# Kernel optimization log

Measured on AMD Instinct MI355X. Metric: run time of the kernel, lower is better.

## Reference

```python
import jax, jax.numpy as jnp
import numpy as np

B, C_IN, H, W = 4, 256, 64, 64
LATENT = 256


def setup_inputs() -> dict:
    key = jax.random.key(0)
    ks = jax.random.split(key, 12)
    s_in = 1.0 / np.sqrt(C_IN)
    s_lat = 1.0 / np.sqrt(LATENT)
    return {
        "x": jax.random.normal(ks[0], (B, C_IN, H, W), dtype=jnp.float32),
        # 1x1 conv weights stored as [out, in]
        "wq": jax.random.normal(ks[1], (LATENT, C_IN), dtype=jnp.float32) * s_in,
        "bq": jnp.zeros((LATENT,), dtype=jnp.float32),
        "wk": jax.random.normal(ks[2], (LATENT, C_IN), dtype=jnp.float32) * s_in,
        "bk": jnp.zeros((LATENT,), dtype=jnp.float32),
        "wv": jax.random.normal(ks[3], (LATENT, C_IN), dtype=jnp.float32) * s_in,
        "bv": jnp.zeros((LATENT,), dtype=jnp.float32),
        "w_out": jax.random.normal(ks[4], (C_IN, LATENT), dtype=jnp.float32) * s_lat,
        "b_out": jnp.zeros((C_IN,), dtype=jnp.float32),
        # positional-embedding MLP (torch nn.Linear: y = x @ W.T + b)
        "mlp_w1": jax.random.normal(ks[5], (LATENT, LATENT), dtype=jnp.float32) * s_lat,
        "mlp_b1": jnp.zeros((LATENT,), dtype=jnp.float32),
        "mlp_w2": jax.random.normal(ks[6], (LATENT, LATENT), dtype=jnp.float32) * s_lat,
        "mlp_b2": jnp.zeros((LATENT,), dtype=jnp.float32),
    }


def _sinusoidal_table(timesteps, dim):
    # embed[t, d] = sin(arg) if d even else cos(arg), arg = t / 10000**(2d/dim)
    t = jnp.arange(timesteps, dtype=jnp.float32)[:, None]
    p = jnp.arange(dim, dtype=jnp.float32)[None, :]
    w = t / jnp.power(jnp.float32(10000.0), 2.0 * p / dim)
    even = (jnp.arange(dim) % 2 == 0)[None, :]
    return jnp.where(even, jnp.sin(w), jnp.cos(w))  # [T, dim]


def _conv1x1(x, w, b):
    # x: [B, Cin, H, W], w: [Cout, Cin]
    return jnp.einsum('bchw,oc->bohw', x, w) + b[None, :, None, None]


def reference(x, wq, bq, wk, bk, wv, bv, w_out, b_out, mlp_w1, mlp_b1, mlp_w2, mlp_b2):
    batch, _, h, w_ = x.shape
    L = wq.shape[0]
    hw = h * w_

    q = _conv1x1(x, wq, bq)
    k = _conv1x1(x, wk, bk)
    v = _conv1x1(x, wv, bv)

    pe = _sinusoidal_table(hw, L)                     # [HW, L]
    pe = jax.nn.silu(pe @ mlp_w1.T + mlp_b1) @ mlp_w2.T + mlp_b2
    pe = pe.reshape(1, L, h, w_)                      # faithful to torch reshape

    q = (q + pe).reshape(batch, L, hw)
    k = (k + pe).reshape(batch, L, hw)
    v = (v + pe).reshape(batch, L, hw)

    # attention[b, i, j] = sum_c q[b, c, i] * k[b, c, j] / sqrt(L)
    att = jnp.einsum('bci,bcj->bij', q, k) / jnp.sqrt(jnp.float32(L))
    att = jax.nn.softmax(att, axis=1)                 # SAGAN-style: softmax over queries
    res = jnp.einsum('bci,bij->bcj', v, att)          # bmm(v, attention)
    res = res.reshape(batch, L, h, w_)
    return _conv1x1(res, w_out, b_out)
```

## Files before the change

kernel.cpp:

```cpp
#include <hip/hip_runtime.h>
#include <cstdint>


typedef short s8v __attribute__((ext_vector_type(8)));
typedef float f32x4 __attribute__((ext_vector_type(4)));
typedef unsigned int u32x2 __attribute__((ext_vector_type(2)));
typedef unsigned int u32x4 __attribute__((ext_vector_type(4)));

#define DEVI static __device__ __forceinline__

DEVI unsigned short f2bf(float f) {
  union { float f; uint32_t u; } x; x.f = f;
  uint32_t u = x.u;
  return (unsigned short)((u + 0x7fffu + ((u >> 16) & 1u)) >> 16);
}

DEVI void pl32swap(uint32_t& a, uint32_t& b) {
#if __has_builtin(__builtin_amdgcn_permlane32_swap)
  u32x2 r = __builtin_amdgcn_permlane32_swap(a, b, false, false);
  a = r[0]; b = r[1];
#else
  asm("v_permlane32_swap_b32 %0, %1" : "+v"(a), "+v"(b));
#endif
}

DEVI void gl_lds16(const void* g, void* l) {
  __builtin_amdgcn_global_load_lds(
      (const __attribute__((address_space(1))) void*)g,
      (__attribute__((address_space(3))) void*)l,
      16, 0, 0);
}

DEVI void stage(const unsigned short* src, int ld, unsigned short* lds, int t) {
  gl_lds16(src + (long)(t >> 2) * ld + (t & 3) * 8, lds + (t >> 6) * 512);
}

template <int OBF, int BIAS, int PEM, int SILU>
__global__ __launch_bounds__(256) void gemm_nt(
    const unsigned short* __restrict__ A, const unsigned short* __restrict__ B,
    void* __restrict__ Cp, int K, int N, int ld, long sA, long sB, long sC,
    const float* __restrict__ bias, const float* __restrict__ pe, float scale) {
  const int bz = blockIdx.z;
  const unsigned short* Ab = A + (long)bz * sA;
  const unsigned short* Bb = B + (long)bz * sB;
  const int m0 = blockIdx.x * 128, n0 = blockIdx.y * 128;
  __shared__ __align__(16) unsigned short As[4096], Bs[4096];
  const int t = threadIdx.x;
  const int wave = t >> 6, lane = t & 63;
  const int wr = wave >> 1, wc = wave & 1;

  f32x4 acc[4][4];
#pragma unroll
  for (int i = 0; i < 4; i++)
#pragma unroll
    for (int j = 0; j < 4; j++) acc[i][j] = f32x4{0.f, 0.f, 0.f, 0.f};

  const int rl = lane & 15, kp = (lane >> 4) * 8;

  for (int k0 = 0; k0 < K; k0 += 32) {
    stage(Ab + (long)m0 * ld + k0, ld, As, t);
    stage(Ab + (long)(m0 + 64) * ld + k0, ld, As + 2048, t);
    stage(Bb + (long)n0 * ld + k0, ld, Bs, t);
    stage(Bb + (long)(n0 + 64) * ld + k0, ld, Bs + 2048, t);
    __syncthreads();

    s8v af[4], bfr[4];
#pragma unroll
    for (int i = 0; i < 4; i++)
      af[i] = *(const s8v*)(As + (wr * 64 + i * 16 + rl) * 32 + kp);
#pragma unroll
    for (int j = 0; j < 4; j++)
      bfr[j] = *(const s8v*)(Bs + (wc * 64 + j * 16 + rl) * 32 + kp);
#pragma unroll
    for (int i = 0; i < 4; i++)
#pragma unroll
      for (int j = 0; j < 4; j++)
        acc[i][j] = __builtin_amdgcn_mfma_f32_16x16x32_bf16(af[i], bfr[j],
                                                            acc[i][j], 0, 0, 0);
    __syncthreads();
  }

  const long cb = (long)bz * sC;
#pragma unroll
  for (int i = 0; i < 4; i++) {
    const int r0 = m0 + wr * 64 + i * 16 + (lane >> 4) * 4;
#pragma unroll
    for (int j = 0; j < 4; j++) {
      const int col = n0 + wc * 64 + j * 16 + (lane & 15);
#pragma unroll
      for (int r = 0; r < 4; r++) {
        const int row = r0 + r;
        float val = acc[i][j][r] * scale;
        if (BIAS == 1) val += bias[row];
        if (BIAS == 2) val += bias[col];
        if (PEM == 1) val += pe[(long)row * 4096 + col];
        if (PEM == 2) val += pe[(long)col * 4096 + row];
        if (SILU) val = val / (1.0f + __expf(-val));
        const long ci = cb + (long)row * N + col;
        if (OBF)
          ((unsigned short*)Cp)[ci] = f2bf(val);
        else
          ((float*)Cp)[ci] = val;
      }
    }
  }
}

__global__ __launch_bounds__(256) void gemm_qk(
    const unsigned short* __restrict__ XT, const unsigned short* __restrict__ wqb,
    const unsigned short* __restrict__ wkb, unsigned short* __restrict__ qT,
    unsigned short* __restrict__ kT, const float* __restrict__ bq,
    const float* __restrict__ bk, const float* __restrict__ pe) {
  const int bz = blockIdx.z;
  const unsigned short* Ab = XT + (long)bz * 1048576;
  const int m0 = blockIdx.x * 128, n0 = blockIdx.y * 128;
  __shared__ __align__(16) unsigned short As[4096], Bq[4096], Bk[4096];
  const int t = threadIdx.x;
  const int wave = t >> 6, lane = t & 63;
  const int wr = wave >> 1, wc = wave & 1;

  f32x4 aq[4][4], ak[4][4];
#pragma unroll
  for (int i = 0; i < 4; i++)
#pragma unroll
    for (int j = 0; j < 4; j++) {
      aq[i][j] = f32x4{0.f, 0.f, 0.f, 0.f};
      ak[i][j] = f32x4{0.f, 0.f, 0.f, 0.f};
    }

  const int rl = lane & 15, kp = (lane >> 4) * 8;

  for (int k0 = 0; k0 < 256; k0 += 32) {
    stage(Ab + (long)m0 * 256 + k0, 256, As, t);
    stage(Ab + (long)(m0 + 64) * 256 + k0, 256, As + 2048, t);
    stage(wqb + (long)n0 * 256 + k0, 256, Bq, t);
    stage(wqb + (long)(n0 + 64) * 256 + k0, 256, Bq + 2048, t);
    stage(wkb + (long)n0 * 256 + k0, 256, Bk, t);
    stage(wkb + (long)(n0 + 64) * 256 + k0, 256, Bk + 2048, t);
    __syncthreads();

    s8v af[4], bq4[4], bk4[4];
#pragma unroll
    for (int i = 0; i < 4; i++)
      af[i] = *(const s8v*)(As + (wr * 64 + i * 16 + rl) * 32 + kp);
#pragma unroll
    for (int j = 0; j < 4; j++) {
      bq4[j] = *(const s8v*)(Bq + (wc * 64 + j * 16 + rl) * 32 + kp);
      bk4[j] = *(const s8v*)(Bk + (wc * 64 + j * 16 + rl) * 32 + kp);
    }
#pragma unroll
    for (int i = 0; i < 4; i++)
#pragma unroll
      for (int j = 0; j < 4; j++) {
        aq[i][j] = __builtin_amdgcn_mfma_f32_16x16x32_bf16(af[i], bq4[j],
                                                           aq[i][j], 0, 0, 0);
        ak[i][j] = __builtin_amdgcn_mfma_f32_16x16x32_bf16(af[i], bk4[j],
                                                           ak[i][j], 0, 0, 0);
      }
    __syncthreads();
  }

  const long cb = (long)bz * 1048576;
#pragma unroll
  for (int i = 0; i < 4; i++) {
    const int r0 = m0 + wr * 64 + i * 16 + (lane >> 4) * 4;
#pragma unroll
    for (int j = 0; j < 4; j++) {
      const int col = n0 + wc * 64 + j * 16 + (lane & 15);
#pragma unroll
      for (int r = 0; r < 4; r++) {
        const int row = r0 + r;
        const float p = pe[(long)col * 4096 + row];
        qT[cb + (long)row * 256 + col] = f2bf(aq[i][j][r] + bq[col] + p);
        kT[cb + (long)row * 256 + col] = f2bf(ak[i][j][r] + bk[col] + p);
      }
    }
  }
}

__global__ __launch_bounds__(256) void gemm_out_f(
    const unsigned short* __restrict__ wob, const float* __restrict__ oPart,
    const float* __restrict__ lPart, const float* __restrict__ bo,
    float* __restrict__ out) {
  const int bz = blockIdx.z;
  const int m0 = blockIdx.x * 128, n0 = blockIdx.y * 128;
  __shared__ __align__(16) unsigned short As[4096], Bs[4096];
  const int t = threadIdx.x;
  const int wave = t >> 6, lane = t & 63;
  const int wr = wave >> 1, wc = wave & 1;

  f32x4 acc[4][4];
#pragma unroll
  for (int i = 0; i < 4; i++)
#pragma unroll
    for (int j = 0; j < 4; j++) acc[i][j] = f32x4{0.f, 0.f, 0.f, 0.f};

  const int rl = lane & 15, kp = (lane >> 4) * 8;
  const int tr = t >> 2, tc8 = (t & 3) * 8;

  const int j0_ = n0 + tr, j1_ = n0 + 64 + tr;
  const float* l0p = lPart + (long)(bz * 2) * 4096;
  const float* l1p = lPart + (long)(bz * 2 + 1) * 4096;
  const float inv0 = 1.0f / (l0p[j0_] + l1p[j0_]);
  const float inv1 = 1.0f / (l0p[j1_] + l1p[j1_]);
  const float* oP0 = oPart + (long)(bz * 2) * 1048576;
  const float* oP1 = oPart + (long)(bz * 2 + 1) * 1048576;

  for (int k0 = 0; k0 < 256; k0 += 32) {
    stage(wob + (long)m0 * 256 + k0, 256, As, t);
    stage(wob + (long)(m0 + 64) * 256 + k0, 256, As + 2048, t);
#pragma unroll
    for (int h = 0; h < 2; h++) {
      const int j = h ? j1_ : j0_;
      const float inv = h ? inv1 : inv0;
      const float4* a4 = (const float4*)(oP0 + (long)j * 256 + k0 + tc8);
      const float4* d4 = (const float4*)(oP1 + (long)j * 256 + k0 + tc8);
      const float4 a0 = a4[0], a1 = a4[1], d0 = d4[0], d1 = d4[1];
      s8v pk;
      pk[0] = (short)f2bf((a0.x + d0.x) * inv);
      pk[1] = (short)f2bf((a0.y + d0.y) * inv);
      pk[2] = (short)f2bf((a0.z + d0.z) * inv);
      pk[3] = (short)f2bf((a0.w + d0.w) * inv);
      pk[4] = (short)f2bf((a1.x + d1.x) * inv);
      pk[5] = (short)f2bf((a1.y + d1.y) * inv);
      pk[6] = (short)f2bf((a1.z + d1.z) * inv);
      pk[7] = (short)f2bf((a1.w + d1.w) * inv);
      *(s8v*)(Bs + h * 2048 + tr * 32 + tc8) = pk;
    }
    __syncthreads();

    s8v af[4], bfr[4];
#pragma unroll
    for (int i = 0; i < 4; i++)
      af[i] = *(const s8v*)(As + (wr * 64 + i * 16 + rl) * 32 + kp);
#pragma unroll
    for (int j = 0; j < 4; j++)
      bfr[j] = *(const s8v*)(Bs + (wc * 64 + j * 16 + rl) * 32 + kp);
#pragma unroll
    for (int i = 0; i < 4; i++)
#pragma unroll
      for (int j = 0; j < 4; j++)
        acc[i][j] = __builtin_amdgcn_mfma_f32_16x16x32_bf16(af[i], bfr[j],
                                                            acc[i][j], 0, 0, 0);
    __syncthreads();
  }

  const long cb = (long)bz * 1048576;
#pragma unroll
  for (int i = 0; i < 4; i++) {
    const int r0 = m0 + wr * 64 + i * 16 + (lane >> 4) * 4;
#pragma unroll
    for (int j = 0; j < 4; j++) {
      const int col = n0 + wc * 64 + j * 16 + (lane & 15);
#pragma unroll
      for (int r = 0; r < 4; r++) {
        const int row = r0 + r;
        out[cb + (long)row * 4096 + col] = acc[i][j][r] + bo[row];
      }
    }
  }
}

__global__ __launch_bounds__(512, 2) void flash_attn(
    const unsigned short* __restrict__ qTp, const unsigned short* __restrict__ kTp,
    const unsigned short* __restrict__ vBp, float* __restrict__ oPart,
    float* __restrict__ lPart) {
  const int bid = blockIdx.x;
  const int xcd = bid & 7;
  const int b = xcd >> 1, ihalf = xcd & 1;
  const int j0 = (bid >> 3) * 128;
  const long S = 1048576;
  const long ibase = (long)ihalf * 2048;
  const unsigned short* q = qTp + (long)b * S;
  const unsigned short* k = kTp + (long)b * S;
  const unsigned short* v = vBp + (long)b * S;
  const int ob = b * 2 + ihalf;

  __shared__ __align__(16) unsigned char ldsb[131584];

  const int t = threadIdx.x;
  const int wave = t >> 6, lane = t & 63;
  const int jq = wave & 3, ch = wave >> 2;
  const int rl = lane & 15, g = lane >> 4;
  const int kp = g * 8;
  const int ksw = ((g ^ ((rl >> 1) & 3)) << 3);
  const int qrow = (rl & 3) | ((rl & 4) << 1) | ((rl & 8) >> 1);
  const int kswq = ((g ^ ((qrow >> 1) & 3)) << 3);
  const int th = t >> 8, tt = t & 255;

  const unsigned short* krow = k + (long)(j0 + jq * 32 + rl) * 256 + kp;
  s8v kreg[2][8];
#pragma unroll
  for (int jf = 0; jf < 2; jf++)
#pragma unroll
    for (int s = 0; s < 8; s++)
      kreg[jf][s] = *(const s8v*)(krow + jf * 16 * 256 + s * 32);

  f32x4 oacc[16][2];
#pragma unroll
  for (int cf = 0; cf < 16; cf++)
#pragma unroll
    for (int jf = 0; jf < 2; jf++) oacc[cf][jf] = f32x4{0.f, 0.f, 0.f, 0.f};
  float plsum[2] = {0.f, 0.f};

  const int tr = tt >> 2, tc = tt & 3;
  const int sc = (tc ^ ((tr >> 1) & 3)) * 8;
  const unsigned short* qsrc[4];
  const unsigned short* vsrc[4];
  const int dsto = (tt >> 6) * 512;
#pragma unroll
  for (int ss = 0; ss < 4; ss++) {
    const int s_ = ss * 2 + th;
    qsrc[ss] = q + ibase * 256 + s_ * 32 + (long)tr * 256 + sc;
    vsrc[ss] = v + (long)((s_ >> 1) * 64) * 4096 + ibase + (s_ & 1) * 32 +
               (long)tr * 4096 + sc;
  }

#define STAGE_QV(bufsel)                                                     \
  {                                                                          \
    unsigned short* qD = (unsigned short*)(ldsb + ((bufsel) << 15));         \
    unsigned short* vD = (unsigned short*)(ldsb + 65536 + ((bufsel) << 15)); \
    _Pragma("unroll") for (int ss = 0; ss < 4; ss++) {                       \
      const int s_ = ss * 2 + th;                                            \
      gl_lds16(qsrc[ss], qD + s_ * 2048 + dsto);                             \
      gl_lds16(vsrc[ss], vD + s_ * 2048 + dsto);                             \
      qsrc[ss] += 16384;                                                     \
      vsrc[ss] += 64;                                                        \
    }                                                                        \
  }

  STAGE_QV(0)

  for (int n = 0; n < 32; ++n) {
    const int cur = n & 1;
    __syncthreads();
    STAGE_QV(cur ^ 1)

    f32x4 sa[2][2];
#pragma unroll
    for (int kk = 0; kk < 2; kk++)
#pragma unroll
      for (int jf = 0; jf < 2; jf++) sa[kk][jf] = f32x4{0.f, 0.f, 0.f, 0.f};
    const unsigned short* qbase =
        (const unsigned short*)(ldsb + (cur << 15)) +
        (ch * 32 + qrow) * 32 + kswq;
#pragma unroll
    for (int s = 0; s < 8; s++) {
      s8v qf0 = *(const s8v*)(qbase + s * 2048);
      s8v qf1 = *(const s8v*)(qbase + s * 2048 + 512);
      sa[0][0] = __builtin_amdgcn_mfma_f32_16x16x32_bf16(qf0, kreg[0][s],
                                                         sa[0][0], 0, 0, 0);
      sa[0][1] = __builtin_amdgcn_mfma_f32_16x16x32_bf16(qf0, kreg[1][s],
                                                         sa[0][1], 0, 0, 0);
      sa[1][0] = __builtin_amdgcn_mfma_f32_16x16x32_bf16(qf1, kreg[0][s],
                                                         sa[1][0], 0, 0, 0);
      sa[1][1] = __builtin_amdgcn_mfma_f32_16x16x32_bf16(qf1, kreg[1][s],
                                                         sa[1][1], 0, 0, 0);
    }

    uint32_t pd[2][2][2];
#pragma unroll
    for (int kk = 0; kk < 2; kk++)
#pragma unroll
      for (int jf = 0; jf < 2; jf++) {
        const float p0 = exp2f(sa[kk][jf][0] * 0.09016844005556021f);
        const float p1 = exp2f(sa[kk][jf][1] * 0.09016844005556021f);
        const float p2 = exp2f(sa[kk][jf][2] * 0.09016844005556021f);
        const float p3 = exp2f(sa[kk][jf][3] * 0.09016844005556021f);
        plsum[jf] += (p0 + p1) + (p2 + p3);
        pd[kk][jf][0] = (uint32_t)f2bf(p0) | ((uint32_t)f2bf(p1) << 16);
        pd[kk][jf][1] = (uint32_t)f2bf(p2) | ((uint32_t)f2bf(p3) << 16);
      }

    s8v pB[2];
#pragma unroll
    for (int jf = 0; jf < 2; jf++) {
      uint32_t a0 = pd[0][jf][0], b0 = pd[1][jf][0];
      uint32_t a1 = pd[0][jf][1], b1 = pd[1][jf][1];
      pl32swap(a0, b0);
      pl32swap(a1, b1);
      u32x4 w4 = {a0, a1, b0, b1};
      pB[jf] = __builtin_bit_cast(s8v, w4);
    }

    const unsigned short* vbase =
        (const unsigned short*)(ldsb + 65536 + (cur << 15)) + ch * 2048 +
        rl * 32 + ksw;
#pragma unroll
    for (int cf = 0; cf < 16; cf++) {
      s8v vb = *(const s8v*)(vbase + (cf >> 2) * 4096 + (cf & 3) * 512);
      oacc[cf][0] = __builtin_amdgcn_mfma_f32_16x16x32_bf16(vb, pB[0],
                                                            oacc[cf][0], 0, 0, 0);
      oacc[cf][1] = __builtin_amdgcn_mfma_f32_16x16x32_bf16(vb, pB[1],
                                                            oacc[cf][1], 0, 0, 0);
    }
  }

#pragma unroll
  for (int jf = 0; jf < 2; jf++) {
    plsum[jf] += __shfl_xor(plsum[jf], 16);
    plsum[jf] += __shfl_xor(plsum[jf], 32);
  }

  __syncthreads();
  float4* ex = (float4*)ldsb;
  float* exl = (float*)(ldsb + 131072);
  if (ch == 1) {
#pragma unroll
    for (int jf = 0; jf < 2; jf++) {
#pragma unroll
      for (int cf = 0; cf < 16; cf++)
        ex[jq * 2048 + (jf * 16 + rl) * 64 + cf * 4 + g] =
            float4{oacc[cf][jf][0], oacc[cf][jf][1], oacc[cf][jf][2],
                   oacc[cf][jf][3]};
      if (g == 0) exl[jq * 32 + jf * 16 + rl] = plsum[jf];
    }
  }
  __syncthreads();
  if (ch == 0) {
    float4* op4 = (float4*)(oPart + (long)ob * 1048576);
#pragma unroll
    for (int jf = 0; jf < 2; jf++) {
      const int jl = jq * 32 + jf * 16 + rl;
      if (g == 0)
        lPart[(long)ob * 4096 + j0 + jl] = plsum[jf] + exl[jl];
#pragma unroll
      for (int cf = 0; cf < 16; cf++) {
        const float4 o = ex[jq * 2048 + (jf * 16 + rl) * 64 + cf * 4 + g];
        op4[(long)(j0 + jl) * 64 + cf * 4 + g] =
            float4{oacc[cf][jf][0] + o.x, oacc[cf][jf][1] + o.y,
                   oacc[cf][jf][2] + o.z, oacc[cf][jf][3] + o.w};
      }
    }
  }
#undef STAGE_QV
}

__global__ __launch_bounds__(256) void convert6(
    const float* __restrict__ a0, const float* __restrict__ a1,
    const float* __restrict__ a2, const float* __restrict__ a3,
    const float* __restrict__ a4, const float* __restrict__ a5,
    unsigned short* __restrict__ dst) {
  int idx = blockIdx.x * 256 + threadIdx.x;
  int m = idx >> 16, r = idx & 65535;
  const float* s;
  switch (m) {
    case 0: s = a0; break;
    case 1: s = a1; break;
    case 2: s = a2; break;
    case 3: s = a3; break;
    case 4: s = a4; break;
    default: s = a5; break;
  }
  dst[idx] = f2bf(s[r]);
}

__global__ __launch_bounds__(256) void embed_k(unsigned short* __restrict__ e) {
  int idx = blockIdx.x * 256 + threadIdx.x;
  int t = idx >> 8, d = idx & 255;
  float freq = exp2f((float)d * -0.10381025296573598f);
  float w = (float)t * freq;
  float s, c;
  __sincosf(w, &s, &c);
  e[idx] = f2bf((d & 1) ? c : s);
}

__global__ void transpose_x(const float* __restrict__ x,
                            unsigned short* __restrict__ xt) {
  __shared__ float tile[32][33];
  const int b = blockIdx.z;
  const int s0 = blockIdx.x * 32, c0 = blockIdx.y * 32;
  const int tx = threadIdx.x, ty = threadIdx.y;
  const float* xb = x + (long)b * 256 * 4096;
#pragma unroll
  for (int r = 0; r < 32; r += 8)
    tile[ty + r][tx] = xb[(long)(c0 + ty + r) * 4096 + s0 + tx];
  __syncthreads();
  unsigned short* xtb = xt + (long)b * 4096 * 256;
#pragma unroll
  for (int r = 0; r < 32; r += 8)
    xtb[(long)(s0 + ty + r) * 256 + c0 + tx] = f2bf(tile[tx][ty + r]);
}

extern "C" void kernel_launch(void* const* d_in, const int* in_sizes, int n_in,
                              void* d_out, int out_size, void* d_ws,
                              size_t ws_size, hipStream_t stream) {
  const float* x  = (const float*)d_in[0];
  const float* wq = (const float*)d_in[1];
  const float* bq = (const float*)d_in[2];
  const float* wk = (const float*)d_in[3];
  const float* bk = (const float*)d_in[4];
  const float* wv = (const float*)d_in[5];
  const float* bv = (const float*)d_in[6];
  const float* wo = (const float*)d_in[7];
  const float* bo = (const float*)d_in[8];
  const float* w1 = (const float*)d_in[9];
  const float* b1 = (const float*)d_in[10];
  const float* w2 = (const float*)d_in[11];
  const float* b2 = (const float*)d_in[12];
  float* out = (float*)d_out;

  char* ws = (char*)d_ws;
  unsigned short* wqb = (unsigned short*)(ws + 0);
  unsigned short* wkb = (unsigned short*)(ws + 131072);
  unsigned short* wvb = (unsigned short*)(ws + 262144);
  unsigned short* wob = (unsigned short*)(ws + 393216);
  unsigned short* w1b = (unsigned short*)(ws + 524288);
  unsigned short* w2b = (unsigned short*)(ws + 655360);
  unsigned short* emb = (unsigned short*)(ws + 786432);
  unsigned short* h1b = (unsigned short*)(ws + 2883584);
  float*          peF = (float*)(ws + 4980736);
  unsigned short* XT  = (unsigned short*)(ws + 9175040);
  unsigned short* qT  = (unsigned short*)(ws + 17563648);
  unsigned short* kT  = (unsigned short*)(ws + 25952256);
  unsigned short* vB  = (unsigned short*)(ws + 34340864);
  float*          oP  = (float*)(ws + 51118080);
  float*          lP  = (float*)(ws + 84672512);
  (void)ws_size; (void)in_sizes; (void)n_in; (void)out_size;

  const dim3 B256(256);
  const long S = 1048576;

  convert6<<<1536, B256, 0, stream>>>(wq, wk, wv, wo, w1, w2, wqb);
  embed_k<<<4096, B256, 0, stream>>>(emb);
  gemm_nt<1, 2, 0, 1><<<dim3(32, 2, 1), B256, 0, stream>>>(
      emb, w1b, h1b, 256, 256, 256, 0, 0, 0, b1, nullptr, 1.0f);
  gemm_nt<0, 2, 0, 0><<<dim3(32, 2, 1), B256, 0, stream>>>(
      h1b, w2b, peF, 256, 256, 256, 0, 0, 0, b2, nullptr, 1.0f);
  transpose_x<<<dim3(128, 8, 4), dim3(32, 8), 0, stream>>>(x, XT);
  gemm_qk<<<dim3(32, 2, 4), B256, 0, stream>>>(XT, wqb, wkb, qT, kT, bq, bk,
                                               peF);
  gemm_nt<1, 1, 1, 0><<<dim3(2, 32, 4), B256, 0, stream>>>(
      wvb, XT, vB, 256, 4096, 256, 0, S, S, bv, peF, 1.0f);

  flash_attn<<<256, dim3(512), 0, stream>>>(qT, kT, vB, oP, lP);

  gemm_out_f<<<dim3(2, 32, 4), B256, 0, stream>>>(wob, oP, lP, bo, out);
}
```

Before: 162.0 us.

## Fuse V projection into QK GEMM and merge prep kernels into one launch

The V projection GEMM now shares the staged X tile with Q and K inside one 512-thread kernel. Each wave computes a 64x32 slice of all three outputs, and V is written transposed with packed ushort4 stores. The weight conversion, sinusoidal embedding and x transpose kernels are merged into one launch that picks its work by block index. This removes redundant reads of X and cuts launch overhead, in exchange for more LDS and register use per block.

```diff
diff --git a/kernel.cpp b/kernel.cpp
--- a/kernel.cpp
+++ b/kernel.cpp
@@ -106,56 +106,62 @@
   }
 }
 
-__global__ __launch_bounds__(256) void gemm_qk(
+__global__ __launch_bounds__(512) void gemm_qkv(
     const unsigned short* __restrict__ XT, const unsigned short* __restrict__ wqb,
-    const unsigned short* __restrict__ wkb, unsigned short* __restrict__ qT,
-    unsigned short* __restrict__ kT, const float* __restrict__ bq,
-    const float* __restrict__ bk, const float* __restrict__ pe) {
+    const unsigned short* __restrict__ wkb, const unsigned short* __restrict__ wvb,
+    unsigned short* __restrict__ qT, unsigned short* __restrict__ kT,
+    unsigned short* __restrict__ vB, const float* __restrict__ bq,
+    const float* __restrict__ bk, const float* __restrict__ bv,
+    const float* __restrict__ pe) {
   const int bz = blockIdx.z;
   const unsigned short* Ab = XT + (long)bz * 1048576;
   const int m0 = blockIdx.x * 128, n0 = blockIdx.y * 128;
-  __shared__ __align__(16) unsigned short As[4096], Bq[4096], Bk[4096];
+  __shared__ __align__(16) unsigned short As[4096], Bq[4096], Bk[4096],
+      Bv[4096];
   const int t = threadIdx.x;
   const int wave = t >> 6, lane = t & 63;
-  const int wr = wave >> 1, wc = wave & 1;
-
-  f32x4 aq[4][4], ak[4][4];
+  const int wm = wave >> 2, wn = wave & 3;
+  const int rl = lane & 15, kp = (lane >> 4) * 8;
+  const int th = t >> 8, tt = t & 255;
+
+  f32x4 aq[4][2], ak[4][2], av[4][2];
 #pragma unroll
   for (int i = 0; i < 4; i++)
 #pragma unroll
-    for (int j = 0; j < 4; j++) {
+    for (int j = 0; j < 2; j++) {
       aq[i][j] = f32x4{0.f, 0.f, 0.f, 0.f};
       ak[i][j] = f32x4{0.f, 0.f, 0.f, 0.f};
-    }
-
-  const int rl = lane & 15, kp = (lane >> 4) * 8;
+      av[i][j] = f32x4{0.f, 0.f, 0.f, 0.f};
+    }
 
   for (int k0 = 0; k0 < 256; k0 += 32) {
-    stage(Ab + (long)m0 * 256 + k0, 256, As, t);
-    stage(Ab + (long)(m0 + 64) * 256 + k0, 256, As + 2048, t);
-    stage(wqb + (long)n0 * 256 + k0, 256, Bq, t);
-    stage(wqb + (long)(n0 + 64) * 256 + k0, 256, Bq + 2048, t);
-    stage(wkb + (long)n0 * 256 + k0, 256, Bk, t);
-    stage(wkb + (long)(n0 + 64) * 256 + k0, 256, Bk + 2048, t);
-    __syncthreads();
-
-    s8v af[4], bq4[4], bk4[4];
+    const long ro = (long)(th * 64) * 256 + k0;
+    stage(Ab + (long)m0 * 256 + ro, 256, As + th * 2048, tt);
+    stage(wqb + (long)n0 * 256 + ro, 256, Bq + th * 2048, tt);
+    stage(wkb + (long)n0 * 256 + ro, 256, Bk + th * 2048, tt);
+    stage(wvb + (long)n0 * 256 + ro, 256, Bv + th * 2048, tt);
+    __syncthreads();
+
+    s8v af[4], b0[2], b1[2], b2[2];
 #pragma unroll
     for (int i = 0; i < 4; i++)
-      af[i] = *(const s8v*)(As + (wr * 64 + i * 16 + rl) * 32 + kp);
-#pragma unroll
-    for (int j = 0; j < 4; j++) {
-      bq4[j] = *(const s8v*)(Bq + (wc * 64 + j * 16 + rl) * 32 + kp);
-      bk4[j] = *(const s8v*)(Bk + (wc * 64 + j * 16 + rl) * 32 + kp);
+      af[i] = *(const s8v*)(As + (wm * 64 + i * 16 + rl) * 32 + kp);
+#pragma unroll
+    for (int j = 0; j < 2; j++) {
+      b0[j] = *(const s8v*)(Bq + (wn * 32 + j * 16 + rl) * 32 + kp);
+      b1[j] = *(const s8v*)(Bk + (wn * 32 + j * 16 + rl) * 32 + kp);
+      b2[j] = *(const s8v*)(Bv + (wn * 32 + j * 16 + rl) * 32 + kp);
     }
 #pragma unroll
     for (int i = 0; i < 4; i++)
 #pragma unroll
-      for (int j = 0; j < 4; j++) {
-        aq[i][j] = __builtin_amdgcn_mfma_f32_16x16x32_bf16(af[i], bq4[j],
+      for (int j = 0; j < 2; j++) {
+        aq[i][j] = __builtin_amdgcn_mfma_f32_16x16x32_bf16(af[i], b0[j],
                                                            aq[i][j], 0, 0, 0);
-        ak[i][j] = __builtin_amdgcn_mfma_f32_16x16x32_bf16(af[i], bk4[j],
+        ak[i][j] = __builtin_amdgcn_mfma_f32_16x16x32_bf16(af[i], b1[j],
                                                            ak[i][j], 0, 0, 0);
+        av[i][j] = __builtin_amdgcn_mfma_f32_16x16x32_bf16(af[i], b2[j],
+                                                           av[i][j], 0, 0, 0);
       }
     __syncthreads();
   }
@@ -163,17 +169,25 @@
   const long cb = (long)bz * 1048576;
 #pragma unroll
   for (int i = 0; i < 4; i++) {
-    const int r0 = m0 + wr * 64 + i * 16 + (lane >> 4) * 4;
-#pragma unroll
-    for (int j = 0; j < 4; j++) {
-      const int col = n0 + wc * 64 + j * 16 + (lane & 15);
+    const int row0 = m0 + wm * 64 + i * 16 + (lane >> 4) * 4;
+#pragma unroll
+    for (int j = 0; j < 2; j++) {
+      const int col = n0 + wn * 32 + j * 16 + rl;
+      const float4 p4 = *(const float4*)(pe + (long)col * 4096 + row0);
+      const float bqc = bq[col], bkc = bk[col], bvc = bv[col];
+      ushort4 vpk;
+      const float pv[4] = {p4.x, p4.y, p4.z, p4.w};
 #pragma unroll
       for (int r = 0; r < 4; r++) {
-        const int row = r0 + r;
-        const float p = pe[(long)col * 4096 + row];
-        qT[cb + (long)row * 256 + col] = f2bf(aq[i][j][r] + bq[col] + p);
-        kT[cb + (long)row * 256 + col] = f2bf(ak[i][j][r] + bk[col] + p);
+        const int row = row0 + r;
+        qT[cb + (long)row * 256 + col] = f2bf(aq[i][j][r] + bqc + pv[r]);
+        kT[cb + (long)row * 256 + col] = f2bf(ak[i][j][r] + bkc + pv[r]);
       }
+      vpk.x = f2bf(av[i][j][0] + bvc + pv[0]);
+      vpk.y = f2bf(av[i][j][1] + bvc + pv[1]);
+      vpk.z = f2bf(av[i][j][2] + bvc + pv[2]);
+      vpk.w = f2bf(av[i][j][3] + bvc + pv[3]);
+      *(ushort4*)(vB + cb + (long)col * 4096 + row0) = vpk;
     }
   }
 }
@@ -436,50 +450,51 @@
 #undef STAGE_QV
 }
 
-__global__ __launch_bounds__(256) void convert6(
+__global__ __launch_bounds__(256) void prep_all(
     const float* __restrict__ a0, const float* __restrict__ a1,
     const float* __restrict__ a2, const float* __restrict__ a3,
     const float* __restrict__ a4, const float* __restrict__ a5,
-    unsigned short* __restrict__ dst) {
-  int idx = blockIdx.x * 256 + threadIdx.x;
-  int m = idx >> 16, r = idx & 65535;
-  const float* s;
-  switch (m) {
-    case 0: s = a0; break;
-    case 1: s = a1; break;
-    case 2: s = a2; break;
-    case 3: s = a3; break;
-    case 4: s = a4; break;
-    default: s = a5; break;
-  }
-  dst[idx] = f2bf(s[r]);
-}
-
-__global__ __launch_bounds__(256) void embed_k(unsigned short* __restrict__ e) {
-  int idx = blockIdx.x * 256 + threadIdx.x;
-  int t = idx >> 8, d = idx & 255;
-  float freq = exp2f((float)d * -0.10381025296573598f);
-  float w = (float)t * freq;
-  float s, c;
-  __sincosf(w, &s, &c);
-  e[idx] = f2bf((d & 1) ? c : s);
-}
-
-__global__ void transpose_x(const float* __restrict__ x,
-                            unsigned short* __restrict__ xt) {
+    unsigned short* __restrict__ wdst, unsigned short* __restrict__ emb,
+    const float* __restrict__ x, unsigned short* __restrict__ xt) {
   __shared__ float tile[32][33];
-  const int b = blockIdx.z;
-  const int s0 = blockIdx.x * 32, c0 = blockIdx.y * 32;
-  const int tx = threadIdx.x, ty = threadIdx.y;
-  const float* xb = x + (long)b * 256 * 4096;
-#pragma unroll
-  for (int r = 0; r < 32; r += 8)
-    tile[ty + r][tx] = xb[(long)(c0 + ty + r) * 4096 + s0 + tx];
-  __syncthreads();
-  unsigned short* xtb = xt + (long)b * 4096 * 256;
-#pragma unroll
-  for (int r = 0; r < 32; r += 8)
-    xtb[(long)(s0 + ty + r) * 256 + c0 + tx] = f2bf(tile[tx][ty + r]);
+  const int bid = blockIdx.x;
+  const int t = threadIdx.x;
+  if (bid < 1536) {
+    int idx = bid * 256 + t;
+    int m = idx >> 16, r = idx & 65535;
+    const float* s;
+    switch (m) {
+      case 0: s = a0; break;
+      case 1: s = a1; break;
+      case 2: s = a2; break;
+      case 3: s = a3; break;
+      case 4: s = a4; break;
+      default: s = a5; break;
+    }
+    wdst[idx] = f2bf(s[r]);
+  } else if (bid < 5632) {
+    int idx = (bid - 1536) * 256 + t;
+    int tt_ = idx >> 8, d = idx & 255;
+    float freq = exp2f((float)d * -0.10381025296573598f);
+    float w = (float)tt_ * freq;
+    float sn, cs;
+    __sincosf(w, &sn, &cs);
+    emb[idx] = f2bf((d & 1) ? cs : sn);
+  } else {
+    const int bid2 = bid - 5632;
+    const int s0 = (bid2 & 127) * 32, c0 = ((bid2 >> 7) & 7) * 32;
+    const int b = bid2 >> 10;
+    const int tx = t & 31, ty = t >> 5;
+    const float* xb = x + (long)b * 256 * 4096;
+#pragma unroll
+    for (int r = 0; r < 32; r += 8)
+      tile[ty + r][tx] = xb[(long)(c0 + ty + r) * 4096 + s0 + tx];
+    __syncthreads();
+    unsigned short* xtb = xt + (long)b * 4096 * 256;
+#pragma unroll
+    for (int r = 0; r < 32; r += 8)
+      xtb[(long)(s0 + ty + r) * 256 + c0 + tx] = f2bf(tile[tx][ty + r]);
+  }
 }
 
 extern "C" void kernel_launch(void* const* d_in, const int* in_sizes, int n_in,
@@ -519,21 +534,14 @@
   (void)ws_size; (void)in_sizes; (void)n_in; (void)out_size;
 
   const dim3 B256(256);
-  const long S = 1048576;
-
-  convert6<<<1536, B256, 0, stream>>>(wq, wk, wv, wo, w1, w2, wqb);
-  embed_k<<<4096, B256, 0, stream>>>(emb);
+
+  prep_all<<<9728, B256, 0, stream>>>(wq, wk, wv, wo, w1, w2, wqb, emb, x, XT);
   gemm_nt<1, 2, 0, 1><<<dim3(32, 2, 1), B256, 0, stream>>>(
       emb, w1b, h1b, 256, 256, 256, 0, 0, 0, b1, nullptr, 1.0f);
   gemm_nt<0, 2, 0, 0><<<dim3(32, 2, 1), B256, 0, stream>>>(
       h1b, w2b, peF, 256, 256, 256, 0, 0, 0, b2, nullptr, 1.0f);
-  transpose_x<<<dim3(128, 8, 4), dim3(32, 8), 0, stream>>>(x, XT);
-  gemm_qk<<<dim3(32, 2, 4), B256, 0, stream>>>(XT, wqb, wkb, qT, kT, bq, bk,
-                                               peF);
-  gemm_nt<1, 1, 1, 0><<<dim3(2, 32, 4), B256, 0, stream>>>(
-      wvb, XT, vB, 256, 4096, 256, 0, S, S, bv, peF, 1.0f);
-
+  gemm_qkv<<<dim3(32, 2, 4), dim3(512), 0, stream>>>(
+      XT, wqb, wkb, wvb, qT, kT, vB, bq, bk, bv, peF);
   flash_attn<<<256, dim3(512), 0, stream>>>(qT, kT, vB, oP, lP);
-
   gemm_out_f<<<dim3(2, 32, 4), B256, 0, stream>>>(wob, oP, lP, bo, out);
 }
```

Result: faster. 148.6 us (-8.3%).
